# Kernel optimization log

Measured on AMD Instinct MI355X. Metric: run time of the kernel, lower is better.

The kernel has to match this reference:

```python
import jax, jax.numpy as jnp
import numpy as np

B, N, F, P = 8, 16384, 128, 28


def setup_inputs() -> dict:
    key = jax.random.key(0)
    k1, k2 = jax.random.split(key)
    x = jax.random.uniform(k1, (B, N, 2), dtype=jnp.float32)  # 2D coords in [0,1]
    sigma = jnp.full((1,), np.log(0.05), dtype=jnp.float32)   # learned log-lengthscale
    image_features = jax.random.normal(k2, (F, P, P), dtype=jnp.float32) / np.sqrt(F)
    return {"x": x, "sigma": sigma, "image_features": image_features}


def reference(x, sigma, image_features):
    # x: [B, N, 2], sigma: [1] (log lengthscale), image_features: [F, P, P]
    P_ = image_features.shape[-1]
    grid = jnp.linspace(0.001, 1.0 - 0.001, P_, dtype=x.dtype)  # [P]
    ls = jnp.exp(sigma[0])                                      # lengthscale
    inv = 0.5 / (ls * ls)
    # pairwise squared dists grid vs each coordinate axis -> [B, P, N]
    d0 = (grid[None, :, None] - x[:, None, :, 0]) ** 2
    d1 = (grid[None, :, None] - x[:, None, :, 1]) ** 2
    k0 = jnp.exp(-inv * d0)  # [B, P, N]
    k1 = jnp.exp(-inv * d1)  # [B, P, N]
    # features[b,n,f] = sum_{p,q} k0[b,p,n] * IF[f,p,q] * k1[b,q,n]
    feats = jnp.einsum('bpn,fpq,bqn->bnf', k0, image_features, k1)
    return feats
```

## Files before the change

kernel.cpp:

```cpp
#include <hip/hip_runtime.h>

#define FDIM  128
#define PDIM  28
#define KPAD  896
#define MPTS  131072
#define BSTR  904

typedef _Float16 half8   __attribute__((ext_vector_type(8)));
typedef _Float16 half4v  __attribute__((ext_vector_type(4)));
typedef float    floatx4 __attribute__((ext_vector_type(4)));

__global__ __launch_bounds__(256) void prep_ift(const float* __restrict__ IF,
                                                _Float16* __restrict__ IFt) {
    int idx = blockIdx.x * 256 + threadIdx.x;
    int f = idx / KPAD;
    int k = idx - f * KPAD;
    int p = k >> 5;
    int q = k & 31;
    float v = (q < PDIM) ? IF[f * (PDIM * PDIM) + p * PDIM + q] : 0.0f;
    IFt[idx] = (_Float16)v;
}

__global__ __launch_bounds__(256, 1) void feats_kernel(
    const float* __restrict__ x,
    const float* __restrict__ sigma,
    const _Float16* __restrict__ IFt,
    float* __restrict__ out)
{
    __shared__ __align__(16) _Float16 bs[64 * BSTR];
    __shared__ _Float16               k0s[128 * 36];
    __shared__ __align__(16) _Float16 k1s[128 * 40];

    const int tid  = threadIdx.x;
    const int lane = tid & 63;
    const int wave = tid >> 6;
    const int ln15 = lane & 15;
    const int quad = lane >> 4;

    const int fs    = blockIdx.x & 1;
    const int mg    = blockIdx.x >> 1;
    const int fbase = fs * 64;

    const float ls    = __expf(sigma[0]);
    const float inv   = 0.5f / (ls * ls);
    const float gstep = 0.998f / 27.0f;

    {
        const int row = tid >> 2;
        const int qtr = tid & 3;
        const uint4* g = (const uint4*)(IFt + (size_t)(fbase + row) * KPAD) + qtr * 28;
        uint4* l = (uint4*)&bs[row * BSTR] + qtr * 28;
        #pragma unroll
        for (int j = 0; j < 28; j++)
            l[j] = g[j];
    }

    const int bfo = (wave * 16 + ln15) * BSTR + quad * 8;

    #pragma unroll 1
    for (int c = 0; c < 8; c++) {
        const int chunkbase = mg * 1024 + c * 128;

        __syncthreads();

        {
            const int ptl = tid & 127;
            const int ptg = chunkbase + ptl;
            if (tid < 128) {
                const float x0 = x[2 * ptg + 0];
                #pragma unroll
                for (int p = 0; p < PDIM; p++) {
                    float d = (0.001f + p * gstep) - x0;
                    k0s[ptl * 36 + p] = (_Float16)__expf(-inv * d * d);
                }
            } else {
                const float x1 = x[2 * ptg + 1];
                #pragma unroll
                for (int q = 0; q < PDIM; q++) {
                    float d = (0.001f + q * gstep) - x1;
                    k1s[ptl * 40 + q] = (_Float16)__expf(-inv * d * d);
                }
                #pragma unroll
                for (int q = PDIM; q < 32; q++)
                    k1s[ptl * 40 + q] = (_Float16)0.0f;
            }
        }
        __syncthreads();

        half8 k1f[8];
        #pragma unroll
        for (int mt = 0; mt < 8; mt++)
            k1f[mt] = *(const half8*)&k1s[(mt * 16 + ln15) * 40 + quad * 8];

        floatx4 acc[8];
        #pragma unroll
        for (int mt = 0; mt < 8; mt++)
            acc[mt] = (floatx4){0.0f, 0.0f, 0.0f, 0.0f};

        #pragma unroll 1
        for (int kk4 = 0; kk4 < 7; kk4++) {
            half4v k0v[8];
            #pragma unroll
            for (int mt = 0; mt < 8; mt++)
                k0v[mt] = *(const half4v*)&k0s[(mt * 16 + ln15) * 36 + kk4 * 4];
            #pragma unroll
            for (int j = 0; j < 4; j++) {
                const half8 bf = *(const half8*)&bs[bfo + (kk4 * 4 + j) * 32];
                #pragma unroll
                for (int mt = 0; mt < 8; mt++) {
                    const half8 af = k1f[mt] * k0v[mt][j];
                    acc[mt] = __builtin_amdgcn_mfma_f32_16x16x32_f16(
                        af, bf, acc[mt], 0, 0, 0);
                }
            }
        }

        const int col = fbase + wave * 16 + ln15;
        #pragma unroll
        for (int mt = 0; mt < 8; mt++) {
            const int row0 = chunkbase + mt * 16 + quad * 4;
            float* op = out + (size_t)row0 * FDIM + col;
            #pragma unroll
            for (int r = 0; r < 4; r++)
                __builtin_nontemporal_store(acc[mt][r], op + (size_t)r * FDIM);
        }
    }
}

extern "C" void kernel_launch(void* const* d_in, const int* in_sizes, int n_in,
                              void* d_out, int out_size, void* d_ws, size_t ws_size,
                              hipStream_t stream) {
    const float* x     = (const float*)d_in[0];
    const float* sigma = (const float*)d_in[1];
    const float* IF    = (const float*)d_in[2];
    float* out = (float*)d_out;

    _Float16* IFt = (_Float16*)d_ws;

    prep_ift<<<(FDIM * KPAD) / 256, 256, 0, stream>>>(IF, IFt);
    feats_kernel<<<256, 256, 0, stream>>>(x, sigma, IFt, out);
}
```

Baseline: 116.0 us.

## Precompute RBF kernels in separate pass and switch to 32x32 MFMA tiles

```diff
diff --git a/kernel.cpp b/kernel.cpp
--- a/kernel.cpp
+++ b/kernel.cpp
@@ -6,9 +6,9 @@
 #define MPTS  131072
 #define BSTR  904
 
-typedef _Float16 half8   __attribute__((ext_vector_type(8)));
-typedef _Float16 half4v  __attribute__((ext_vector_type(4)));
-typedef float    floatx4 __attribute__((ext_vector_type(4)));
+typedef _Float16 half8    __attribute__((ext_vector_type(8)));
+typedef _Float16 half4v   __attribute__((ext_vector_type(4)));
+typedef float    floatx16 __attribute__((ext_vector_type(16)));
 
 __global__ __launch_bounds__(256) void prep_ift(const float* __restrict__ IF,
                                                 _Float16* __restrict__ IFt) {
@@ -21,108 +21,131 @@
     IFt[idx] = (_Float16)v;
 }
 
-__global__ __launch_bounds__(256, 1) void feats_kernel(
-    const float* __restrict__ x,
-    const float* __restrict__ sigma,
+__global__ __launch_bounds__(256) void prep_k(const float* __restrict__ x,
+                                              const float* __restrict__ sigma,
+                                              _Float16* __restrict__ k0t,
+                                              _Float16* __restrict__ k1t) {
+    const int pt = blockIdx.x * 256 + threadIdx.x;
+    const float ls    = __expf(sigma[0]);
+    const float inv   = 0.5f / (ls * ls);
+    const float gstep = 0.998f / 27.0f;
+    const float x0 = x[2 * pt + 0];
+    const float x1 = x[2 * pt + 1];
+
+    _Float16 k0[28], k1[32];
+    #pragma unroll
+    for (int p = 0; p < PDIM; p++) {
+        float d = (0.001f + p * gstep) - x0;
+        k0[p] = (_Float16)__expf(-inv * d * d);
+    }
+    #pragma unroll
+    for (int q = 0; q < PDIM; q++) {
+        float d = (0.001f + q * gstep) - x1;
+        k1[q] = (_Float16)__expf(-inv * d * d);
+    }
+    #pragma unroll
+    for (int q = PDIM; q < 32; q++) k1[q] = (_Float16)0.0f;
+
+    #pragma unroll
+    for (int p4 = 0; p4 < 7; p4++) {
+        half4v v; 
+        #pragma unroll
+        for (int i = 0; i < 4; i++) v[i] = k0[p4 * 4 + i];
+        *(half4v*)&k0t[((size_t)p4 * MPTS + pt) * 4] = v;
+    }
+    #pragma unroll
+    for (int h = 0; h < 4; h++) {
+        half8 v;
+        #pragma unroll
+        for (int j = 0; j < 8; j++) v[j] = k1[h * 8 + j];
+        *(half8*)&k1t[((size_t)h * MPTS + pt) * 8] = v;
+    }
+}
+
+__global__ __launch_bounds__(256, 2) void feats_kernel(
     const _Float16* __restrict__ IFt,
+    const _Float16* __restrict__ k0t,
+    const _Float16* __restrict__ k1t,
     float* __restrict__ out)
 {
-    __shared__ __align__(16) _Float16 bs[64 * BSTR];
-    __shared__ _Float16               k0s[128 * 36];
-    __shared__ __align__(16) _Float16 k1s[128 * 40];
+    __shared__ __align__(16) _Float16 bs[32 * BSTR];
 
     const int tid  = threadIdx.x;
     const int lane = tid & 63;
     const int wave = tid >> 6;
-    const int ln15 = lane & 15;
-    const int quad = lane >> 4;
+    const int ln31 = lane & 31;
+    const int g    = lane >> 5;
 
-    const int fs    = blockIdx.x & 1;
-    const int mg    = blockIdx.x >> 1;
-    const int fbase = fs * 64;
-
-    const float ls    = __expf(sigma[0]);
-    const float inv   = 0.5f / (ls * ls);
-    const float gstep = 0.998f / 27.0f;
+    const int fs    = blockIdx.x & 3;
+    const int pg    = blockIdx.x >> 2;
+    const int fbase = fs * 32;
 
     {
-        const int row = tid >> 2;
-        const int qtr = tid & 3;
-        const uint4* g = (const uint4*)(IFt + (size_t)(fbase + row) * KPAD) + qtr * 28;
-        uint4* l = (uint4*)&bs[row * BSTR] + qtr * 28;
+        const int row = tid >> 3;
+        const int seg = tid & 7;
+        const uint4* gsrc = (const uint4*)(IFt + (size_t)(fbase + row) * KPAD);
+        uint4* ldst = (uint4*)&bs[row * BSTR];
         #pragma unroll
-        for (int j = 0; j < 28; j++)
-            l[j] = g[j];
+        for (int j = 0; j < 14; j++)
+            ldst[seg * 14 + j] = gsrc[seg * 14 + j];
     }
+    __syncthreads();
 
-    const int bfo = (wave * 16 + ln15) * BSTR + quad * 8;
+    const int bfo = ln31 * BSTR + g * 8;
 
     #pragma unroll 1
-    for (int c = 0; c < 8; c++) {
-        const int chunkbase = mg * 1024 + c * 128;
+    for (int c = 0; c < 2; c++) {
+        const int chunkbase = pg * 1024 + c * 512 + wave * 128;
 
-        __syncthreads();
+        half4v k0v[4][7];
+        half8  k1f[4][2];
+        #pragma unroll
+        for (int mt = 0; mt < 4; mt++) {
+            const int ptr_ = chunkbase + mt * 32 + ln31;
+            #pragma unroll
+            for (int p4 = 0; p4 < 7; p4++)
+                k0v[mt][p4] = *(const half4v*)&k0t[((size_t)p4 * MPTS + ptr_) * 4];
+            k1f[mt][0] = *(const half8*)&k1t[((size_t)(0 + g) * MPTS + ptr_) * 8];
+            k1f[mt][1] = *(const half8*)&k1t[((size_t)(2 + g) * MPTS + ptr_) * 8];
+        }
 
-        {
-            const int ptl = tid & 127;
-            const int ptg = chunkbase + ptl;
-            if (tid < 128) {
-                const float x0 = x[2 * ptg + 0];
+        floatx16 acc[4];
+        #pragma unroll
+        for (int mt = 0; mt < 4; mt++)
+            #pragma unroll
+            for (int r = 0; r < 16; r++) acc[mt][r] = 0.0f;
+
+        #pragma unroll
+        for (int p4 = 0; p4 < 7; p4++) {
+            #pragma unroll
+            for (int pj = 0; pj < 4; pj++) {
+                const int p = p4 * 4 + pj;
+                const half8 bf0 = *(const half8*)&bs[bfo + p * 32];
+                const half8 bf1 = *(const half8*)&bs[bfo + p * 32 + 16];
                 #pragma unroll
-                for (int p = 0; p < PDIM; p++) {
-                    float d = (0.001f + p * gstep) - x0;
-                    k0s[ptl * 36 + p] = (_Float16)__expf(-inv * d * d);
-                }
-            } else {
-                const float x1 = x[2 * ptg + 1];
-                #pragma unroll
-                for (int q = 0; q < PDIM; q++) {
-                    float d = (0.001f + q * gstep) - x1;
-                    k1s[ptl * 40 + q] = (_Float16)__expf(-inv * d * d);
+                for (int mt = 0; mt < 4; mt++) {
+                    const half8 af = k1f[mt][0] * k0v[mt][p4][pj];
+                    acc[mt] = __builtin_amdgcn_mfma_f32_32x32x16_f16(
+                        af, bf0, acc[mt], 0, 0, 0);
                 }
                 #pragma unroll
-                for (int q = PDIM; q < 32; q++)
-                    k1s[ptl * 40 + q] = (_Float16)0.0f;
-            }
-        }
-        __syncthreads();
-
-        half8 k1f[8];
-        #pragma unroll
-        for (int mt = 0; mt < 8; mt++)
-            k1f[mt] = *(const half8*)&k1s[(mt * 16 + ln15) * 40 + quad * 8];
-
-        floatx4 acc[8];
-        #pragma unroll
-        for (int mt = 0; mt < 8; mt++)
-            acc[mt] = (floatx4){0.0f, 0.0f, 0.0f, 0.0f};
-
-        #pragma unroll 1
-        for (int kk4 = 0; kk4 < 7; kk4++) {
-            half4v k0v[8];
-            #pragma unroll
-            for (int mt = 0; mt < 8; mt++)
-                k0v[mt] = *(const half4v*)&k0s[(mt * 16 + ln15) * 36 + kk4 * 4];
-            #pragma unroll
-            for (int j = 0; j < 4; j++) {
-                const half8 bf = *(const half8*)&bs[bfo + (kk4 * 4 + j) * 32];
-                #pragma unroll
-                for (int mt = 0; mt < 8; mt++) {
-                    const half8 af = k1f[mt] * k0v[mt][j];
-                    acc[mt] = __builtin_amdgcn_mfma_f32_16x16x32_f16(
-                        af, bf, acc[mt], 0, 0, 0);
+                for (int mt = 0; mt < 4; mt++) {
+                    const half8 af = k1f[mt][1] * k0v[mt][p4][pj];
+                    acc[mt] = __builtin_amdgcn_mfma_f32_32x32x16_f16(
+                        af, bf1, acc[mt], 0, 0, 0);
                 }
             }
         }
 
-        const int col = fbase + wave * 16 + ln15;
         #pragma unroll
-        for (int mt = 0; mt < 8; mt++) {
-            const int row0 = chunkbase + mt * 16 + quad * 4;
-            float* op = out + (size_t)row0 * FDIM + col;
+        for (int mt = 0; mt < 4; mt++) {
             #pragma unroll
-            for (int r = 0; r < 4; r++)
-                __builtin_nontemporal_store(acc[mt][r], op + (size_t)r * FDIM);
+            for (int reg = 0; reg < 16; reg++) {
+                const int row = (reg & 3) + 8 * (reg >> 2) + 4 * g;
+                const size_t prow = (size_t)(chunkbase + mt * 32 + row);
+                __builtin_nontemporal_store(acc[mt][reg],
+                                            out + prow * FDIM + fbase + ln31);
+            }
         }
     }
 }
@@ -136,7 +159,10 @@
     float* out = (float*)d_out;
 
     _Float16* IFt = (_Float16*)d_ws;
+    _Float16* k0t = (_Float16*)((char*)d_ws + (256 << 10));
+    _Float16* k1t = (_Float16*)((char*)d_ws + (256 << 10) + 7340032);
 
     prep_ift<<<(FDIM * KPAD) / 256, 256, 0, stream>>>(IF, IFt);
-    feats_kernel<<<256, 256, 0, stream>>>(x, sigma, IFt, out);
+    prep_k<<<MPTS / 256, 256, 0, stream>>>(x, sigma, k0t, k1t);
+    feats_kernel<<<512, 256, 0, stream>>>(IFt, k0t, k1t, out);
 }
```

New measurement: 156.3 us. +34.8%, slower.
